# Kernel tuning notes

Measured on AMD Instinct MI355X. Metric: run time of the kernel, lower is better.

The kernel has to match this reference:

```python
import jax, jax.numpy as jnp
import numpy as np

B, Q, D = 8, 900, 256
NH, DH = 8, 32
FF = 1024
NLEVELS, NPOINTS, NLAYERS = 4, 4, 6
SHAPES = [(100, 100), (50, 50), (25, 25), (13, 13)]
S = sum(h * w for h, w in SHAPES)  # 13294
EPS = 1e-5
SCALE = 1.0 / float(np.sqrt(DH))


def layer_norm(x, g, b):
    mu = jnp.mean(x, -1, keepdims=True)
    var = jnp.var(x, -1, keepdims=True)
    return (x - mu) * jax.lax.rsqrt(var + EPS) * g + b


def mha(x, wi, bi, wo, bo):
    qkv = x @ wi.T + bi
    q, k, v = jnp.split(qkv, 3, axis=-1)
    q = q.reshape(B, Q, NH, DH)
    k = k.reshape(B, Q, NH, DH)
    v = v.reshape(B, Q, NH, DH)
    attn = jax.nn.softmax(jnp.einsum('bqhd,bkhd->bhqk', q, k) * SCALE, -1)
    o = jnp.einsum('bhqk,bkhd->bqhd', attn, v).reshape(B, Q, D)
    return o @ wo.T + bo


def msda_core(value, loc, aw):
    # value (B,S,NH,DH); loc (B,Q,NH,L,P,2) in [0,1]; aw (B,Q,NH,L,P)
    v = value.transpose(0, 2, 1, 3)  # (B,NH,S,DH)
    out = jnp.zeros((B, NH, Q, DH), value.dtype)
    start = 0
    for lvl, (H_, W_) in enumerate(SHAPES):
        vl = v[:, :, start:start + H_ * W_]  # (B,NH,HW,DH)
        start += H_ * W_
        l = loc[:, :, :, lvl].transpose(0, 2, 1, 3, 4).reshape(B, NH, Q * NPOINTS, 2)
        # grid_sample align_corners=False pixel coords
        x = l[..., 0] * W_ - 0.5
        y = l[..., 1] * H_ - 0.5
        x0 = jnp.floor(x)
        y0 = jnp.floor(y)
        wx = x - x0
        wy = y - y0
        g = jnp.zeros((B, NH, Q * NPOINTS, DH), value.dtype)
        for dy, dx, w in ((0, 0, (1 - wx) * (1 - wy)), (0, 1, wx * (1 - wy)),
                          (1, 0, (1 - wx) * wy), (1, 1, wx * wy)):
            xi = x0 + dx
            yi = y0 + dy
            valid = ((xi >= 0) & (xi < W_) & (yi >= 0) & (yi < H_)).astype(value.dtype)
            idx = (jnp.clip(yi, 0, H_ - 1) * W_ + jnp.clip(xi, 0, W_ - 1)).astype(jnp.int32)
            gi = jnp.take_along_axis(vl, idx[..., None], axis=2)  # (B,NH,QP,DH)
            g = g + gi * (w * valid)[..., None]
        g = g.reshape(B, NH, Q, NPOINTS, DH)
        a = aw[:, :, :, lvl].transpose(0, 2, 1, 3)  # (B,NH,Q,P)
        out = out + jnp.einsum('bhqpd,bhqp->bhqd', g, a)
    return out.transpose(0, 2, 1, 3).reshape(B, Q, D)


def msda(query, ref, value_in, vp_w, vp_b, so_w, so_b, aw_w, aw_b, op_w, op_b):
    value = (value_in @ vp_w.T + vp_b).reshape(B, S, NH, DH)
    off = (query @ so_w.T + so_b).reshape(B, Q, NH, NLEVELS, NPOINTS, 2)
    aw = (query @ aw_w.T + aw_b).reshape(B, Q, NH, NLEVELS * NPOINTS)
    aw = jax.nn.softmax(aw, -1).reshape(B, Q, NH, NLEVELS, NPOINTS)
    # offset normalizer is (W, H) per level
    norm = jnp.array([[w, h] for h, w in SHAPES], jnp.float32)
    loc = ref[:, :, None, :, None, :] + off / norm[None, None, None, :, None, :]
    return msda_core(value, loc, aw) @ op_w.T + op_b


def setup_inputs():
    key = jax.random.key(0)
    it = iter(jax.random.split(key, 32))

    def rn(shape, s=0.02):
        return jax.random.normal(next(it), shape, jnp.float32) * s

    z = lambda n: jnp.zeros((n,), jnp.float32)
    o = lambda n: jnp.ones((n,), jnp.float32)
    NOFF = NH * NLEVELS * NPOINTS
    return {
        'tgt': rn((B, Q, D), 1.0),
        'reference_points': jax.random.uniform(next(it), (B, Q, 2), jnp.float32),
        'memory': rn((B, S, D), 1.0),
        'spatial_shapes': jnp.array(SHAPES, jnp.int32),
        'level_start_index': jnp.array(np.cumsum([0] + [h * w for h, w in SHAPES[:-1]]), jnp.int32),
        'valid_ratios': jnp.ones((B, NLEVELS, 2), jnp.float32),
        'query_pos': rn((B, Q, D), 1.0),
        'sa_in_w': rn((3 * D, D)), 'sa_in_b': z(3 * D),
        'sa_out_w': rn((D, D)), 'sa_out_b': z(D),
        'n1_g': o(D), 'n1_b': z(D),
        'n2_g': o(D), 'n2_b': z(D),
        'n3_g': o(D), 'n3_b': z(D),
        'vp_w': rn((D, D)), 'vp_b': z(D),
        'so_w': rn((NOFF * 2, D)), 'so_b': rn((NOFF * 2,), 0.5),
        'aw_w': rn((NOFF, D)), 'aw_b': z(NOFF),
        'op_w': rn((D, D)), 'op_b': z(D),
        'ff1_w': rn((FF, D)), 'ff1_b': z(FF),
        'ff2_w': rn((D, FF)), 'ff2_b': z(D),
    }


def reference(tgt, reference_points, memory, spatial_shapes, level_start_index,
              valid_ratios, query_pos,
              sa_in_w, sa_in_b, sa_out_w, sa_out_b,
              n1_g, n1_b, n2_g, n2_b, n3_g, n3_b,
              vp_w, vp_b, so_w, so_b, aw_w, aw_b, op_w, op_b,
              ff1_w, ff1_b, ff2_w, ff2_b):
    # NOTE: nn.ModuleList([decoder_layer]*num_layers) in the source shares one
    # layer's weights across all 6 layers; bbox_embed is None so reference
    # points are constant across layers.
    output = tgt
    ref_input = reference_points[:, :, None, :] * valid_ratios[:, None, :, :]  # (B,Q,L,2)
    inter, inter_refs = [], []
    for _ in range(NLAYERS):
        output = output + query_pos
        t2 = mha(output, sa_in_w, sa_in_b, sa_out_w, sa_out_b)
        output = layer_norm(output + t2, n1_g, n1_b)
        t2 = msda(output, ref_input, memory, vp_w, vp_b, so_w, so_b, aw_w, aw_b, op_w, op_b)
        output = layer_norm(output + t2, n2_g, n2_b)
        t2 = jax.nn.relu(output @ ff1_w.T + ff1_b) @ ff2_w.T + ff2_b
        output = layer_norm(output + t2, n3_g, n3_b)
        inter.append(output)
        inter_refs.append(reference_points)
    return (jnp.stack(inter), jnp.stack(inter_refs))
```

## Files before the change

kernel.cpp:

```cpp
#include <hip/hip_runtime.h>
#include <hip/hip_bf16.h>

typedef __hip_bfloat16 bf16;
typedef __bf16 bf16x8 __attribute__((ext_vector_type(8)));
typedef float  f32x4  __attribute__((ext_vector_type(4)));

#define NB 8
#define NQ 900
#define DM 256
#define NHEADS 8
#define DHEAD 32
#define NFF 1024
#define NLAY 6
#define NS 13294
#define BQ (NB*NQ)
#define LN_EPS 1e-5f
#define ATT_SCALE 0.17677669529663687f
#define SAK 40
#define VWS 264

__device__ __forceinline__ float bfd(const bf16* p, size_t i){ return __bfloat162float(p[i]); }

__device__ __forceinline__ float ldv(const void* p, size_t i, int mode, bool extF32)
{
    if (mode == 0) return ((const float*)p)[i];
    if (mode == 1) return bfd((const bf16*)p, i);
    return extF32 ? ((const float*)p)[i] : bfd((const bf16*)p, i);
}

__device__ __forceinline__ void unpack8(uint4 u, float* t)
{
    t[0] = __uint_as_float((u.x & 0xffffu) << 16);
    t[1] = __uint_as_float(u.x & 0xffff0000u);
    t[2] = __uint_as_float((u.y & 0xffffu) << 16);
    t[3] = __uint_as_float(u.y & 0xffff0000u);
    t[4] = __uint_as_float((u.z & 0xffffu) << 16);
    t[5] = __uint_as_float(u.z & 0xffff0000u);
    t[6] = __uint_as_float((u.w & 0xffffu) << 16);
    t[7] = __uint_as_float(u.w & 0xffff0000u);
}

__global__ __launch_bounds__(256) void detect_dtype(const void* __restrict__ tgt,
        float* __restrict__ flag)
{
    __shared__ float red[256];
    int t = threadIdx.x;
    const unsigned short* u = (const unsigned short*)tgt;
    float m = 0.f;
    for (int i = t; i < 2048; i += 256) {
        unsigned int bits = ((unsigned int)u[i]) << 16;
        float v = fabsf(__uint_as_float(bits));
        if (!isfinite(v)) v = 1e30f;
        m = fmaxf(m, v);
    }
    red[t] = m;
    __syncthreads();
    for (int st = 128; st; st >>= 1) {
        if (t < st) red[t] = fmaxf(red[t], red[t + st]);
        __syncthreads();
    }
    if (t == 0) flag[0] = (red[0] > 1e8f) ? 1.f : 0.f;
}

__global__ __launch_bounds__(256) void convert_w(const void* __restrict__ src,
        bf16* __restrict__ dst, const float* __restrict__ flagp)
{
    const bool ef = flagp[0] > 0.5f;
    size_t base = ((size_t)blockIdx.x * 256 + threadIdx.x) * 8;
    if (ef) {
        const float* s = (const float*)src + base;
        float4 f0 = *(const float4*)s;
        float4 f1 = *(const float4*)(s + 4);
        union { bf16 a[8]; uint4 u; } t;
        t.a[0] = __float2bfloat16(f0.x); t.a[1] = __float2bfloat16(f0.y);
        t.a[2] = __float2bfloat16(f0.z); t.a[3] = __float2bfloat16(f0.w);
        t.a[4] = __float2bfloat16(f1.x); t.a[5] = __float2bfloat16(f1.y);
        t.a[6] = __float2bfloat16(f1.z); t.a[7] = __float2bfloat16(f1.w);
        *(uint4*)(dst + base) = t.u;
    } else {
        *(uint4*)(dst + base) = *(const uint4*)((const bf16*)src + base);
    }
}

__global__ __launch_bounds__(256) void gemm_vp(const void* __restrict__ A,
        const bf16* __restrict__ Wb, const void* __restrict__ bias,
        bf16* __restrict__ C, int M, const float* __restrict__ flagp)
{
    const bool ef = flagp[0] > 0.5f;
    __shared__ __align__(16) bf16 Wl[256 * VWS];
    __shared__ __align__(16) bf16 Al[32 * VWS];
    const int tid = threadIdx.x;
    const int w = tid >> 6, lane = tid & 63, lm = lane & 15, lq = lane >> 4;
    const int wq = w * 64;

    for (int u = tid; u < 8192; u += 256) {
        int row = u >> 5, col = (u & 31) * 8;
        *(uint4*)&Wl[row * VWS + col] = *(const uint4*)(Wb + (size_t)row * 256 + col);
    }

    float bv[4];
    #pragma unroll
    for (int nt = 0; nt < 4; nt++) bv[nt] = ldv(bias, wq + nt * 16 + lm, 2, ef);

    const int arow_l = tid >> 3;
    const int acol   = (tid & 7) * 32;

    const int ntiles = (M + 31) / 32;
    for (int tile = blockIdx.x; tile < ntiles; tile += gridDim.x) {
        const int m0 = tile * 32;
        __syncthreads();
        {
            const int grow = m0 + arow_l;
            if (grow < M) {
                if (ef) {
                    const float* ap = (const float*)A + (size_t)grow * 256 + acol;
                    #pragma unroll
                    for (int j = 0; j < 4; j++) {
                        float4 f0 = *(const float4*)(ap + j * 8);
                        float4 f1 = *(const float4*)(ap + j * 8 + 4);
                        union { bf16 a[8]; uint4 u; } t;
                        t.a[0] = __float2bfloat16(f0.x); t.a[1] = __float2bfloat16(f0.y);
                        t.a[2] = __float2bfloat16(f0.z); t.a[3] = __float2bfloat16(f0.w);
                        t.a[4] = __float2bfloat16(f1.x); t.a[5] = __float2bfloat16(f1.y);
                        t.a[6] = __float2bfloat16(f1.z); t.a[7] = __float2bfloat16(f1.w);
                        *(uint4*)&Al[arow_l * VWS + acol + j * 8] = t.u;
                    }
                } else {
                    const bf16* ap = (const bf16*)A + (size_t)grow * 256 + acol;
                    #pragma unroll
                    for (int j = 0; j < 4; j++)
                        *(uint4*)&Al[arow_l * VWS + acol + j * 8] =
                            *(const uint4*)(ap + j * 8);
                }
            } else {
                uint4 z = make_uint4(0u, 0u, 0u, 0u);
                #pragma unroll
                for (int j = 0; j < 4; j++)
                    *(uint4*)&Al[arow_l * VWS + acol + j * 8] = z;
            }
        }
        __syncthreads();

        f32x4 acc[2][4];
        #pragma unroll
        for (int mi = 0; mi < 2; mi++)
            #pragma unroll
            for (int nt = 0; nt < 4; nt++)
                acc[mi][nt] = (f32x4){0.f, 0.f, 0.f, 0.f};

        #pragma unroll
        for (int ks = 0; ks < 8; ks++) {
            bf16x8 af[2];
            #pragma unroll
            for (int mi = 0; mi < 2; mi++)
                af[mi] = *(const bf16x8*)&Al[(mi * 16 + lm) * VWS + ks * 32 + lq * 8];
            #pragma unroll
            for (int nt = 0; nt < 4; nt++) {
                bf16x8 bfr = *(const bf16x8*)&Wl[(wq + nt * 16 + lm) * VWS + ks * 32 + lq * 8];
                #pragma unroll
                for (int mi = 0; mi < 2; mi++)
                    acc[mi][nt] = __builtin_amdgcn_mfma_f32_16x16x32_bf16(
                                      af[mi], bfr, acc[mi][nt], 0, 0, 0);
            }
        }

        #pragma unroll
        for (int mi = 0; mi < 2; mi++) {
            #pragma unroll
            for (int r = 0; r < 4; r++) {
                int m = m0 + mi * 16 + lq * 4 + r;
                if (m >= M) continue;
                #pragma unroll
                for (int nt = 0; nt < 4; nt++) {
                    int col = wq + nt * 16 + lm;
                    C[(size_t)m * 256 + col] = __float2bfloat16(acc[mi][nt][r] + bv[nt]);
                }
            }
        }
    }
}

__device__ __forceinline__ void stage_a32(bf16* As, const void* A, bool a_bf16,
        int m0, int M, int K, int k0, int tid)
{
    const int row = tid >> 3, col = (tid & 7) * 4;
    const int arow = m0 + row;
    union { bf16 a[4]; uint2 u; } t;
    if (arow < M) {
        size_t base = (size_t)arow * K + k0 + col;
        if (a_bf16) {
            t.u = *(const uint2*)((const bf16*)A + base);
        } else {
            float4 f = *(const float4*)((const float*)A + base);
            t.a[0] = __float2bfloat16(f.x); t.a[1] = __float2bfloat16(f.y);
            t.a[2] = __float2bfloat16(f.z); t.a[3] = __float2bfloat16(f.w);
        }
    } else {
        t.u = make_uint2(0u, 0u);
    }
    *(uint2*)&As[row * SAK + col] = t.u;
}

__global__ __launch_bounds__(256) void gemm_a(const void* __restrict__ A, int amode,
        const bf16* __restrict__ Wb, const void* __restrict__ bias,
        void* __restrict__ C, int cmode, int M, int N, int K, int relu,
        const float* __restrict__ flagp)
{
    const bool ef = flagp[0] > 0.5f;
    const bool a_bf16 = (amode == 1) || (amode == 2 && !ef);
    __shared__ __align__(16) bf16 As[32 * SAK];
    __shared__ __align__(16) bf16 Ws[256 * SAK];
    const int tid = threadIdx.x;
    const int m0 = blockIdx.y * 32, n0 = blockIdx.x * 256;
    const int w = tid >> 6, lane = tid & 63, lm = lane & 15, lq = lane >> 4;
    const int wr = w >> 1, wc = w & 1;
    const int srow = tid >> 2, scol = (tid & 3) * 8;

    f32x4 acc[8];
    #pragma unroll
    for (int nt = 0; nt < 8; nt++) acc[nt] = (f32x4){0.f, 0.f, 0.f, 0.f};

    for (int k0 = 0; k0 < K; k0 += 32) {
        stage_a32(As, A, a_bf16, m0, M, K, k0, tid);
        #pragma unroll
        for (int it = 0; it < 4; it++) {
            int rr = it * 64 + srow;
            *(uint4*)&Ws[rr * SAK + scol] =
                *(const uint4*)(Wb + (size_t)(n0 + rr) * K + k0 + scol);
        }
        __syncthreads();

        bf16x8 af = *(const bf16x8*)&As[(wr * 16 + lm) * SAK + lq * 8];
        #pragma unroll
        for (int nt = 0; nt < 8; nt++) {
            bf16x8 bfr = *(const bf16x8*)&Ws[(wc * 128 + nt * 16 + lm) * SAK + lq * 8];
            acc[nt] = __builtin_amdgcn_mfma_f32_16x16x32_bf16(af, bfr, acc[nt], 0, 0, 0);
        }
        __syncthreads();
    }

    #pragma unroll
    for (int nt = 0; nt < 8; nt++) {
        int n = n0 + wc * 128 + nt * 16 + lm;
        float bv = ldv(bias, n, 2, ef);
        #pragma unroll
        for (int r = 0; r < 4; r++) {
            int m = m0 + wr * 16 + lq * 4 + r;
            if (m >= M) continue;
            float v = acc[nt][r] + bv;
            if (relu) v = fmaxf(v, 0.f);
            size_t ci = (size_t)m * N + n;
            if (cmode == 0) ((float*)C)[ci] = v;
            else            ((bf16*)C)[ci] = __float2bfloat16(v);
        }
    }
}

__global__ __launch_bounds__(256) void gemm_ln(const bf16* __restrict__ A,
        const bf16* __restrict__ Wb, const void* __restrict__ bias,
        const float* __restrict__ res, const void* __restrict__ gw,
        const void* __restrict__ bw, float* __restrict__ out32,
        bf16* __restrict__ outbf, void* __restrict__ dout, size_t obase,
        const void* __restrict__ qp, int M, int K,
        const float* __restrict__ flagp)
{
    const bool ef = flagp[0] > 0.5f;
    __shared__ __align__(16) bf16 As[32 * SAK];
    __shared__ __align__(16) bf16 Ws[256 * SAK];
    const int tid = threadIdx.x;
    const int m0 = blockIdx.y * 32;
    const int w = tid >> 6, lane = tid & 63, lm = lane & 15, lq = lane >> 4;
    const int wr = w >> 1, wc = w & 1;
    const int srow = tid >> 2, scol = (tid & 3) * 8;

    f32x4 acc[8];
    #pragma unroll
    for (int nt = 0; nt < 8; nt++) acc[nt] = (f32x4){0.f, 0.f, 0.f, 0.f};

    for (int k0 = 0; k0 < K; k0 += 32) {
        stage_a32(As, A, true, m0, M, K, k0, tid);
        #pragma unroll
        for (int it = 0; it < 4; it++) {
            int rr = it * 64 + srow;
            *(uint4*)&Ws[rr * SAK + scol] =
                *(const uint4*)(Wb + (size_t)rr * K + k0 + scol);
        }
        __syncthreads();

        bf16x8 af = *(const bf16x8*)&As[(wr * 16 + lm) * SAK + lq * 8];
        #pragma unroll
        for (int nt = 0; nt < 8; nt++) {
            bf16x8 bfr = *(const bf16x8*)&Ws[(wc * 128 + nt * 16 + lm) * SAK + lq * 8];
            acc[nt] = __builtin_amdgcn_mfma_f32_16x16x32_bf16(af, bfr, acc[nt], 0, 0, 0);
        }
        __syncthreads();
    }

    float bias_c[8], gcol[8], bcol[8];
    #pragma unroll
    for (int nt = 0; nt < 8; nt++) {
        int col = wc * 128 + nt * 16 + lm;
        bias_c[nt] = ldv(bias, col, 2, ef);
        gcol[nt]   = ldv(gw,   col, 2, ef);
        bcol[nt]   = ldv(bw,   col, 2, ef);
    }
    #pragma unroll
    for (int r = 0; r < 4; r++) {
        int row = m0 + wr * 16 + lq * 4 + r;
        bool vr_ = row < M;
        #pragma unroll
        for (int nt = 0; nt < 8; nt++) {
            int col = wc * 128 + nt * 16 + lm;
            float rv = vr_ ? res[(size_t)row * DM + col] : 0.f;
            acc[nt][r] += bias_c[nt] + rv;
        }
    }

    float* red = (float*)As;
    float mu[4], rstd[4];
    #pragma unroll
    for (int r = 0; r < 4; r++) {
        float s = 0.f;
        #pragma unroll
        for (int nt = 0; nt < 8; nt++) s += acc[nt][r];
        s += __shfl_xor(s, 1, 64); s += __shfl_xor(s, 2, 64);
        s += __shfl_xor(s, 4, 64); s += __shfl_xor(s, 8, 64);
        if (lm == 0) red[(wr * 16 + lq * 4 + r) * 2 + wc] = s;
    }
    __syncthreads();
    #pragma unroll
    for (int r = 0; r < 4; r++) {
        int rl = wr * 16 + lq * 4 + r;
        mu[r] = (red[rl * 2] + red[rl * 2 + 1]) * (1.f / DM);
    }
    #pragma unroll
    for (int r = 0; r < 4; r++) {
        float q = 0.f;
        #pragma unroll
        for (int nt = 0; nt < 8; nt++) {
            float d = acc[nt][r] - mu[r];
            q += d * d;
        }
        q += __shfl_xor(q, 1, 64); q += __shfl_xor(q, 2, 64);
        q += __shfl_xor(q, 4, 64); q += __shfl_xor(q, 8, 64);
        if (lm == 0) red[64 + (wr * 16 + lq * 4 + r) * 2 + wc] = q;
    }
    __syncthreads();
    #pragma unroll
    for (int r = 0; r < 4; r++) {
        int rl = wr * 16 + lq * 4 + r;
        float var = (red[64 + rl * 2] + red[64 + rl * 2 + 1]) * (1.f / DM);
        rstd[r] = rsqrtf(var + LN_EPS);
    }

    #pragma unroll
    for (int r = 0; r < 4; r++) {
        int row = m0 + wr * 16 + lq * 4 + r;
        if (row >= M) continue;
        size_t rbase = (size_t)row * DM;
        #pragma unroll
        for (int nt = 0; nt < 8; nt++) {
            int col = wc * 128 + nt * 16 + lm;
            float o = (acc[nt][r] - mu[r]) * rstd[r] * gcol[nt] + bcol[nt];
            if (dout) {
                if (ef) ((float*)dout)[obase + rbase + col] = o;
                else    ((bf16*)dout)[obase + rbase + col] = __float2bfloat16(o);
            }
            float o2 = o + (qp ? ldv(qp, rbase + col, 2, ef) : 0.f);
            out32[rbase + col] = o2;
            outbf[rbase + col] = __float2bfloat16(o2);
        }
    }
}

__global__ __launch_bounds__(256) void gemm_soaw(const bf16* __restrict__ A,
        const bf16* __restrict__ Wb, const void* __restrict__ b1,
        const void* __restrict__ b2, float* __restrict__ C1,
        float* __restrict__ C2, int M, const float* __restrict__ flagp)
{
    const bool ef = flagp[0] > 0.5f;
    const int K = DM;
    __shared__ __align__(16) bf16 As[32 * SAK];
    __shared__ __align__(16) bf16 Ws[128 * SAK];
    const int tid = threadIdx.x;
    const int m0 = blockIdx.y * 32, n0 = blockIdx.x * 128;
    const int w = tid >> 6, lane = tid & 63, lm = lane & 15, lq = lane >> 4;
    const int wr = w >> 1, wc = w & 1;
    const int srow = tid >> 2, scol = (tid & 3) * 8;

    f32x4 acc[4];
    #pragma unroll
    for (int nt = 0; nt < 4; nt++) acc[nt] = (f32x4){0.f, 0.f, 0.f, 0.f};

    for (int k0 = 0; k0 < K; k0 += 32) {
        stage_a32(As, A, true, m0, M, K, k0, tid);
        #pragma unroll
        for (int it = 0; it < 2; it++) {
            int rr = it * 64 + srow;
            *(uint4*)&Ws[rr * SAK + scol] =
                *(const uint4*)(Wb + (size_t)(n0 + rr) * K + k0 + scol);
        }
        __syncthreads();

        bf16x8 af = *(const bf16x8*)&As[(wr * 16 + lm) * SAK + lq * 8];
        #pragma unroll
        for (int nt = 0; nt < 4; nt++) {
            bf16x8 bfr = *(const bf16x8*)&Ws[(wc * 64 + nt * 16 + lm) * SAK + lq * 8];
            acc[nt] = __builtin_amdgcn_mfma_f32_16x16x32_bf16(af, bfr, acc[nt], 0, 0, 0);
        }
        __syncthreads();
    }

    float* Cd; const void* bsrc; int nst, c0;
    if (n0 < 256) { Cd = C1; bsrc = b1; nst = 256; c0 = n0; }
    else          { Cd = C2; bsrc = b2; nst = 128; c0 = n0 - 256; }

    #pragma unroll
    for (int nt = 0; nt < 4; nt++) {
        int cl = wc * 64 + nt * 16 + lm;
        float bv = ldv(bsrc, c0 + cl, 2, ef);
        #pragma unroll
        for (int r = 0; r < 4; r++) {
            int m = m0 + wr * 16 + lq * 4 + r;
            if (m >= M) continue;
            Cd[(size_t)m * nst + c0 + cl] = acc[nt][r] + bv;
        }
    }
}

__global__ __launch_bounds__(256) void add_qpos(const void* __restrict__ a, int amode,
        const void* __restrict__ qp, float* __restrict__ o, bf16* __restrict__ ob,
        const float* __restrict__ flagp)
{
    const bool ef = flagp[0] > 0.5f;
    int i = blockIdx.x * 256 + threadIdx.x;
    float v = ldv(a, i, amode, ef) + ldv(qp, i, 2, ef);
    o[i]  = v;
    ob[i] = __float2bfloat16(v);
}

__global__ __launch_bounds__(256) void mha_mfma(const bf16* __restrict__ qkv,
        bf16* __restrict__ out)
{
    const int qt = blockIdx.x, h = blockIdx.y, b = blockIdx.z;
    const int q0 = qt * 64;
    const int tid = threadIdx.x;
    const int w = tid >> 6, lane = tid & 63;
    const int lm = lane & 15, lq = lane >> 4;
    const int srow = tid >> 2, sc = (tid & 3) * 8;

    __shared__ __align__(16) bf16 Qs[64][SAK];
    __shared__ __align__(16) bf16 Ks[64][SAK];
    __shared__ __align__(16) bf16 Vt[32][66];
    __shared__ __align__(16) bf16 Pt[64][66];

    const bf16* base = qkv + (size_t)b * NQ * 768;

    {
        bf16 tmp[8];
        if (q0 + srow < NQ) {
            uint4 u = *(const uint4*)(base + (size_t)(q0 + srow) * 768 + h * DHEAD + sc);
            float t[8]; unpack8(u, t);
            #pragma unroll
            for (int i = 0; i < 8; i++) tmp[i] = __float2bfloat16(t[i] * ATT_SCALE);
        } else {
            #pragma unroll
            for (int i = 0; i < 8; i++) tmp[i] = __float2bfloat16(0.f);
        }
        *(uint4*)&Qs[srow][sc] = *(const uint4*)tmp;
    }
    __syncthreads();
    const bf16x8 qf = *(const bf16x8*)&Qs[w * 16 + lm][lq * 8];

    f32x4 O[2] = {{0.f,0.f,0.f,0.f},{0.f,0.f,0.f,0.f}};
    float mrow = -1e30f, lrow = 0.f;

    for (int k0 = 0; k0 < NQ; k0 += 64) {
        __syncthreads();
        {
            uint4 uk = {0u,0u,0u,0u}, uv = {0u,0u,0u,0u};
            if (k0 + srow < NQ) {
                const bf16* rp = base + (size_t)(k0 + srow) * 768 + h * DHEAD + sc;
                uk = *(const uint4*)(rp + 256);
                uv = *(const uint4*)(rp + 512);
            }
            *(uint4*)&Ks[srow][sc] = uk;
            const bf16* vv = (const bf16*)&uv;
            #pragma unroll
            for (int i = 0; i < 8; i++) Vt[sc + i][srow] = vv[i];
        }
        __syncthreads();

        float sv[16];
        #pragma unroll
        for (int mt = 0; mt < 4; mt++) {
            bf16x8 kf = *(const bf16x8*)&Ks[mt * 16 + lm][lq * 8];
            f32x4 d = __builtin_amdgcn_mfma_f32_16x16x32_bf16(kf, qf,
                        (f32x4){0.f,0.f,0.f,0.f}, 0, 0, 0);
            sv[mt*4+0] = d[0]; sv[mt*4+1] = d[1]; sv[mt*4+2] = d[2]; sv[mt*4+3] = d[3];
        }
        #pragma unroll
        for (int mt = 0; mt < 4; mt++)
            #pragma unroll
            for (int r = 0; r < 4; r++)
                if (k0 + mt * 16 + lq * 4 + r >= NQ) sv[mt*4+r] = -1e30f;

        float tmax = sv[0];
        #pragma unroll
        for (int j = 1; j < 16; j++) tmax = fmaxf(tmax, sv[j]);
        tmax = fmaxf(tmax, __shfl_xor(tmax, 16, 64));
        tmax = fmaxf(tmax, __shfl_xor(tmax, 32, 64));
        float mnew = fmaxf(mrow, tmax);
        float alpha = __expf(mrow - mnew);
        mrow = mnew;
        float psum = 0.f;
        #pragma unroll
        for (int j = 0; j < 16; j++) {
            float p = __expf(sv[j] - mnew);
            sv[j] = p; psum += p;
        }
        psum += __shfl_xor(psum, 16, 64);
        psum += __shfl_xor(psum, 32, 64);
        lrow = lrow * alpha + psum;

        #pragma unroll
        for (int mt = 0; mt < 4; mt++)
            #pragma unroll
            for (int r = 0; r < 4; r++)
                Pt[mt * 16 + lq * 4 + r][w * 16 + lm] = __float2bfloat16(sv[mt*4+r]);

        #pragma unroll
        for (int mt = 0; mt < 2; mt++)
            #pragma unroll
            for (int r = 0; r < 4; r++) O[mt][r] *= alpha;
        #pragma unroll
        for (int ks = 0; ks < 2; ks++) {
            union { bf16 a[8]; bf16x8 v; } pf;
            #pragma unroll
            for (int j = 0; j < 8; j++)
                pf.a[j] = Pt[ks * 32 + lq * 8 + j][w * 16 + lm];
            #pragma unroll
            for (int mt = 0; mt < 2; mt++) {
                bf16x8 vf = *(const bf16x8*)&Vt[mt * 16 + lm][ks * 32 + lq * 8];
                O[mt] = __builtin_amdgcn_mfma_f32_16x16x32_bf16(vf, pf.v, O[mt], 0, 0, 0);
            }
        }
    }

    int q = q0 + w * 16 + lm;
    if (q < NQ) {
        float invl = 1.f / lrow;
        bf16* op = out + ((size_t)(b * NQ + q)) * DM + h * DHEAD;
        #pragma unroll
        for (int mt = 0; mt < 2; mt++)
            #pragma unroll
            for (int r = 0; r < 4; r++)
                op[mt * 16 + lq * 4 + r] = __float2bfloat16(O[mt][r] * invl);
    }
}

__global__ __launch_bounds__(256) void msda_sample(const bf16* __restrict__ value,
        const float* __restrict__ off, const float* __restrict__ aw,
        const void* __restrict__ refp, const void* __restrict__ vr,
        bf16* __restrict__ out, const float* __restrict__ flagp)
{
    const bool ef = flagp[0] > 0.5f;
    int bq = blockIdx.x; int b = bq / NQ;
    int tid = threadIdx.x; int h = tid >> 5, d = tid & 31;
    __shared__ float sOff[256];
    __shared__ float sAw[128];
    __shared__ float sref[2];
    __shared__ float svr[8];
    sOff[tid] = off[(size_t)bq * 256 + tid];
    if (tid < 128) sAw[tid] = aw[(size_t)bq * 128 + tid];
    if (tid < 2)   sref[tid] = ldv(refp, bq * 2 + tid, 2, ef);
    if (tid < 8)   svr[tid]  = ldv(vr, b * 8 + tid, 2, ef);
    __syncthreads();
    if (tid < 8) {
        float* p = &sAw[tid * 16];
        float mx = -1e30f;
        #pragma unroll
        for (int j = 0; j < 16; j++) mx = fmaxf(mx, p[j]);
        float s = 0.f;
        #pragma unroll
        for (int j = 0; j < 16; j++) { float e = __expf(p[j] - mx); p[j] = e; s += e; }
        float inv = 1.f / s;
        #pragma unroll
        for (int j = 0; j < 16; j++) p[j] *= inv;
    }
    __syncthreads();
    const bf16* vb = value + (size_t)b * NS * DM + h * DHEAD + d;
    const int HS[4] = {100, 50, 25, 13};
    const int ST[4] = {0, 10000, 12500, 13125};
    float acc = 0.f;
    #pragma unroll
    for (int lvl = 0; lvl < 4; lvl++) {
        int W_ = HS[lvl], H_ = HS[lvl], st = ST[lvl];
        float rx = sref[0] * svr[lvl*2 + 0] * (float)W_;
        float ry = sref[1] * svr[lvl*2 + 1] * (float)H_;
        #pragma unroll
        for (int p = 0; p < 4; p++) {
            int oi = h * 32 + lvl * 8 + p * 2;
            float x = fminf(fmaxf(rx + sOff[oi]     - 0.5f, -4.f), (float)W_ + 4.f);
            float y = fminf(fmaxf(ry + sOff[oi + 1] - 0.5f, -4.f), (float)H_ + 4.f);
            float x0f = floorf(x), y0f = floorf(y);
            float wx = x - x0f, wy = y - y0f;
            int x0 = (int)x0f, y0 = (int)y0f;
            int x1i = x0 + 1, y1i = y0 + 1;
            bool vx0 = (x0 >= 0) && (x0 < W_), vx1 = (x1i >= 0) && (x1i < W_);
            bool vy0 = (y0 >= 0) && (y0 < H_), vy1 = (y1i >= 0) && (y1i < H_);
            float g = 0.f;
            if (vy0) {
                int rowo = (st + y0 * W_) * DM;
                if (vx0) g += (1.f - wx) * (1.f - wy) * __bfloat162float(vb[rowo + x0  * DM]);
                if (vx1) g += wx         * (1.f - wy) * __bfloat162float(vb[rowo + x1i * DM]);
            }
            if (vy1) {
                int rowo = (st + y1i * W_) * DM;
                if (vx0) g += (1.f - wx) * wy * __bfloat162float(vb[rowo + x0  * DM]);
                if (vx1) g += wx         * wy * __bfloat162float(vb[rowo + x1i * DM]);
            }
            acc += g * sAw[h * 16 + lvl * 4 + p];
        }
    }
    out[(size_t)bq * DM + tid] = __float2bfloat16(acc);
}

__global__ __launch_bounds__(256) void copy_refs(const void* __restrict__ refp,
        void* __restrict__ out, const float* __restrict__ flagp)
{
    const bool ef = flagp[0] > 0.5f;
    int i = blockIdx.x * 256 + threadIdx.x;
    if (i >= NLAY * BQ * 2) return;
    float v = ldv(refp, i % (BQ * 2), 2, ef);
    size_t oi = (size_t)NLAY * BQ * DM + i;
    if (ef) ((float*)out)[oi] = v;
    else    ((bf16*)out)[oi] = __float2bfloat16(v);
}

extern "C" void kernel_launch(void* const* d_in, const int* in_sizes, int n_in,
                              void* d_out, int out_size, void* d_ws, size_t ws_size,
                              hipStream_t stream)
{
    const void* tgt     = d_in[0];
    const void* refp    = d_in[1];
    const void* memory  = d_in[2];
    const void* vr      = d_in[5];
    const void* qp      = d_in[6];
    const void* sa_in_w = d_in[7];
    const void* sa_in_b = d_in[8];
    const void* sa_out_w= d_in[9];
    const void* sa_out_b= d_in[10];
    const void* n1_g    = d_in[11];
    const void* n1_b    = d_in[12];
    const void* n2_g    = d_in[13];
    const void* n2_b    = d_in[14];
    const void* n3_g    = d_in[15];
    const void* n3_b    = d_in[16];
    const void* vp_w    = d_in[17];
    const void* vp_b    = d_in[18];
    const void* so_w    = d_in[19];
    const void* so_b    = d_in[20];
    const void* aw_w    = d_in[21];
    const void* aw_b    = d_in[22];
    const void* op_w    = d_in[23];
    const void* op_b    = d_in[24];
    const void* ff1_w   = d_in[25];
    const void* ff1_b   = d_in[26];
    const void* ff2_w   = d_in[27];
    const void* ff2_b   = d_in[28];

    char* w = (char*)d_ws;
    float* flagp  = (float*)w;  w += 256;
    bf16*  value  = (bf16*)w;   w += (size_t)NB * NS * DM * 2;
    float* outbuf = (float*)w;  w += (size_t)BQ * DM * 4;
    float* x1samp = (float*)w;  w += (size_t)BQ * DM * 4;
    bf16*  bigb   = (bf16*)w;   w += (size_t)BQ * NFF * 2;
    float* attoff = (float*)w;  w += (size_t)BQ * DM * 4;
    float* awb    = (float*)w;  w += (size_t)BQ * 128 * 4;
    bf16*  abuf   = (bf16*)w;   w += (size_t)BQ * DM * 2;
    bf16*  outbf  = (bf16*)w;   w += (size_t)BQ * DM * 2;
    bf16* wb_sa_in = (bf16*)w;  w += (size_t)768 * 256 * 2;
    bf16* wb_sa_out= (bf16*)w;  w += (size_t)256 * 256 * 2;
    bf16* wb_soaw  = (bf16*)w;  w += (size_t)384 * 256 * 2;
    bf16* wb_op    = (bf16*)w;  w += (size_t)256 * 256 * 2;
    bf16* wb_ff1   = (bf16*)w;  w += (size_t)NFF * 256 * 2;
    bf16* wb_ff2   = (bf16*)w;  w += (size_t)256 * NFF * 2;
    bf16* wb_vp    = (bf16*)w;  w += (size_t)256 * 256 * 2;

    const int gy = (BQ + 31) / 32;
    const int MV = NB * NS;

    detect_dtype<<<1, 256, 0, stream>>>(tgt, flagp);
    convert_w<<< 96, 256, 0, stream>>>(sa_in_w,  wb_sa_in,  flagp);
    convert_w<<< 32, 256, 0, stream>>>(sa_out_w, wb_sa_out, flagp);
    convert_w<<< 32, 256, 0, stream>>>(so_w,     wb_soaw,   flagp);
    convert_w<<< 16, 256, 0, stream>>>(aw_w,     wb_soaw + 256 * 256, flagp);
    convert_w<<< 32, 256, 0, stream>>>(op_w,     wb_op,     flagp);
    convert_w<<<128, 256, 0, stream>>>(ff1_w,    wb_ff1,    flagp);
    convert_w<<<128, 256, 0, stream>>>(ff2_w,    wb_ff2,    flagp);
    convert_w<<< 32, 256, 0, stream>>>(vp_w,     wb_vp,     flagp);

    gemm_vp<<<256, 256, 0, stream>>>(memory, wb_vp, vp_b, value, MV, flagp);

    copy_refs<<<(NLAY * BQ * 2 + 255) / 256, 256, 0, stream>>>(refp, d_out, flagp);

    add_qpos<<<BQ * DM / 256, 256, 0, stream>>>(tgt, 2, qp, x1samp, abuf, flagp);

    for (int l = 0; l < NLAY; l++) {
        gemm_a<<<dim3(768/256, gy), 256, 0, stream>>>(
            abuf, 1, wb_sa_in, sa_in_b, bigb, 1, BQ, 768, DM, 0, flagp);
        mha_mfma<<<dim3(15, NHEADS, NB), 256, 0, stream>>>(bigb, abuf);
        gemm_ln<<<dim3(1, gy), 256, 0, stream>>>(
            abuf, wb_sa_out, sa_out_b, x1samp, n1_g, n1_b,
            outbuf, outbf, nullptr, 0, nullptr, BQ, DM, flagp);

        gemm_soaw<<<dim3(3, gy), 256, 0, stream>>>(
            outbf, wb_soaw, so_b, aw_b, attoff, awb, BQ, flagp);
        msda_sample<<<BQ, 256, 0, stream>>>(value, attoff, awb, refp, vr, abuf, flagp);
        gemm_ln<<<dim3(1, gy), 256, 0, stream>>>(
            abuf, wb_op, op_b, outbuf, n2_g, n2_b,
            outbuf, outbf, nullptr, 0, nullptr, BQ, DM, flagp);

        gemm_a<<<dim3(NFF/256, gy), 256, 0, stream>>>(
            outbf, 1, wb_ff1, ff1_b, bigb, 1, BQ, NFF, DM, 1, flagp);
        gemm_ln<<<dim3(1, gy), 256, 0, stream>>>(
            bigb, wb_ff2, ff2_b, outbuf, n3_g, n3_b,
            x1samp, abuf, d_out, (size_t)l * BQ * DM, qp, BQ, NFF, flagp);
    }
}
```

Before: 1.722 ms.

## Vectorize MSDA sampling with 8-channel loads and 8 queries per block

Rewrites the deformable-attention sampling kernel so that each thread handles 8 contiguous channels through 16-byte bf16 loads rather than one scalar channel. Each block now processes 8 queries, 32 threads per query, and stages the offsets and attention weights with float4 loads. The aim is fewer memory instructions for the gather and less per-block overhead, since the old launch used one block per query. The trade-off is more registers per thread and fewer threads in flight to hide gather latency. It also relies on an unpack8 helper and assumes BQ is divisible by 8, which holds here.

```diff
diff --git a/kernel.cpp b/kernel.cpp
--- a/kernel.cpp
+++ b/kernel.cpp
@@ -559,25 +559,41 @@
     }
 }
 
-__global__ __launch_bounds__(256) void msda_sample(const bf16* __restrict__ value,
+__global__ __launch_bounds__(256) void msda_sample8(const bf16* __restrict__ value,
         const float* __restrict__ off, const float* __restrict__ aw,
         const void* __restrict__ refp, const void* __restrict__ vr,
         bf16* __restrict__ out, const float* __restrict__ flagp)
 {
     const bool ef = flagp[0] > 0.5f;
-    int bq = blockIdx.x; int b = bq / NQ;
-    int tid = threadIdx.x; int h = tid >> 5, d = tid & 31;
-    __shared__ float sOff[256];
-    __shared__ float sAw[128];
-    __shared__ float sref[2];
-    __shared__ float svr[8];
-    sOff[tid] = off[(size_t)bq * 256 + tid];
-    if (tid < 128) sAw[tid] = aw[(size_t)bq * 128 + tid];
-    if (tid < 2)   sref[tid] = ldv(refp, bq * 2 + tid, 2, ef);
-    if (tid < 8)   svr[tid]  = ldv(vr, b * 8 + tid, 2, ef);
+    const int tid = threadIdx.x;
+    const int bq0 = blockIdx.x * 8;
+
+    __shared__ float sOff[8][256];
+    __shared__ float sAw[8][128];
+    __shared__ float sref[8][2];
+    __shared__ float svrq[8][8];
+
+    {
+        const float* osrc = off + (size_t)bq0 * 256;
+        #pragma unroll
+        for (int i = 0; i < 2; i++) {
+            int e = i * 1024 + tid * 4;
+            *(float4*)&sOff[e >> 8][e & 255] = *(const float4*)(osrc + e);
+        }
+        int e2 = tid * 4;
+        *(float4*)&sAw[e2 >> 7][e2 & 127] = *(const float4*)(aw + (size_t)bq0 * 128 + e2);
+    }
+    if (tid < 16) sref[tid >> 1][tid & 1] = ldv(refp, (size_t)(bq0 + (tid >> 1)) * 2 + (tid & 1), 2, ef);
+    if (tid < 64) {
+        int qi = tid >> 3, j = tid & 7;
+        int b = (bq0 + qi) / NQ;
+        svrq[qi][j] = ldv(vr, b * 8 + j, 2, ef);
+    }
     __syncthreads();
-    if (tid < 8) {
-        float* p = &sAw[tid * 16];
+
+    if (tid < 64) {
+        int qi = tid >> 3, h = tid & 7;
+        float* p = &sAw[qi][h * 16];
         float mx = -1e30f;
         #pragma unroll
         for (int j = 0; j < 16; j++) mx = fmaxf(mx, p[j]);
@@ -589,41 +605,83 @@
         for (int j = 0; j < 16; j++) p[j] *= inv;
     }
     __syncthreads();
-    const bf16* vb = value + (size_t)b * NS * DM + h * DHEAD + d;
+
+    const int qi = tid >> 5, sub = tid & 31;
+    const int h = sub >> 2, cg = sub & 3;
+    const int bq = bq0 + qi;
+    const int b = bq / NQ;
+    const bf16* vb = value + (size_t)b * NS * DM + h * DHEAD + cg * 8;
+
+    float acc[8];
+    #pragma unroll
+    for (int j = 0; j < 8; j++) acc[j] = 0.f;
+
     const int HS[4] = {100, 50, 25, 13};
     const int ST[4] = {0, 10000, 12500, 13125};
-    float acc = 0.f;
     #pragma unroll
     for (int lvl = 0; lvl < 4; lvl++) {
-        int W_ = HS[lvl], H_ = HS[lvl], st = ST[lvl];
-        float rx = sref[0] * svr[lvl*2 + 0] * (float)W_;
-        float ry = sref[1] * svr[lvl*2 + 1] * (float)H_;
+        const int W_ = HS[lvl], H_ = HS[lvl], st = ST[lvl];
+        float rx = sref[qi][0] * svrq[qi][lvl * 2 + 0] * (float)W_;
+        float ry = sref[qi][1] * svrq[qi][lvl * 2 + 1] * (float)H_;
         #pragma unroll
         for (int p = 0; p < 4; p++) {
             int oi = h * 32 + lvl * 8 + p * 2;
-            float x = fminf(fmaxf(rx + sOff[oi]     - 0.5f, -4.f), (float)W_ + 4.f);
-            float y = fminf(fmaxf(ry + sOff[oi + 1] - 0.5f, -4.f), (float)H_ + 4.f);
+            float x = fminf(fmaxf(rx + sOff[qi][oi]     - 0.5f, -4.f), (float)W_ + 4.f);
+            float y = fminf(fmaxf(ry + sOff[qi][oi + 1] - 0.5f, -4.f), (float)H_ + 4.f);
             float x0f = floorf(x), y0f = floorf(y);
             float wx = x - x0f, wy = y - y0f;
             int x0 = (int)x0f, y0 = (int)y0f;
             int x1i = x0 + 1, y1i = y0 + 1;
             bool vx0 = (x0 >= 0) && (x0 < W_), vx1 = (x1i >= 0) && (x1i < W_);
             bool vy0 = (y0 >= 0) && (y0 < H_), vy1 = (y1i >= 0) && (y1i < H_);
-            float g = 0.f;
+            float g[8];
+            #pragma unroll
+            for (int j = 0; j < 8; j++) g[j] = 0.f;
+            float t[8];
             if (vy0) {
                 int rowo = (st + y0 * W_) * DM;
-                if (vx0) g += (1.f - wx) * (1.f - wy) * __bfloat162float(vb[rowo + x0  * DM]);
-                if (vx1) g += wx         * (1.f - wy) * __bfloat162float(vb[rowo + x1i * DM]);
+                if (vx0) {
+                    uint4 u = *(const uint4*)(vb + rowo + x0 * DM);
+                    unpack8(u, t);
+                    float wgt = (1.f - wx) * (1.f - wy);
+                    #pragma unroll
+                    for (int j = 0; j < 8; j++) g[j] += wgt * t[j];
+                }
+                if (vx1) {
+                    uint4 u = *(const uint4*)(vb + rowo + x1i * DM);
+                    unpack8(u, t);
+                    float wgt = wx * (1.f - wy);
+                    #pragma unroll
+                    for (int j = 0; j < 8; j++) g[j] += wgt * t[j];
+                }
             }
             if (vy1) {
                 int rowo = (st + y1i * W_) * DM;
-                if (vx0) g += (1.f - wx) * wy * __bfloat162float(vb[rowo + x0  * DM]);
-                if (vx1) g += wx         * wy * __bfloat162float(vb[rowo + x1i * DM]);
+                if (vx0) {
+                    uint4 u = *(const uint4*)(vb + rowo + x0 * DM);
+                    unpack8(u, t);
+                    float wgt = (1.f - wx) * wy;
+                    #pragma unroll
+                    for (int j = 0; j < 8; j++) g[j] += wgt * t[j];
+                }
+                if (vx1) {
+                    uint4 u = *(const uint4*)(vb + rowo + x1i * DM);
+                    unpack8(u, t);
+                    float wgt = wx * wy;
+                    #pragma unroll
+                    for (int j = 0; j < 8; j++) g[j] += wgt * t[j];
+                }
             }
-            acc += g * sAw[h * 16 + lvl * 4 + p];
-        }
-    }
-    out[(size_t)bq * DM + tid] = __float2bfloat16(acc);
+            float a = sAw[qi][h * 16 + lvl * 4 + p];
+            #pragma unroll
+            for (int j = 0; j < 8; j++) acc[j] += a * g[j];
+        }
+    }
+
+    union { bf16 t[8]; uint4 u; } pk;
+    #pragma unroll
+    for (int j = 0; j < 8; j++) pk.t[j] = __float2bfloat16(acc[j]);
+    *(uint4*)(out + (size_t)bq * DM + h * DHEAD + cg * 8) = pk.u;
 }
 
 __global__ __launch_bounds__(256) void copy_refs(const void* __restrict__ refp,
@@ -717,7 +775,7 @@
 
         gemm_soaw<<<dim3(3, gy), 256, 0, stream>>>(
             outbf, wb_soaw, so_b, aw_b, attoff, awb, BQ, flagp);
-        msda_sample<<<BQ, 256, 0, stream>>>(value, attoff, awb, refp, vr, abuf, flagp);
+        msda_sample8<<<BQ / 8, 256, 0, stream>>>(value, attoff, awb, refp, vr, abuf, flagp);
         gemm_ln<<<dim3(1, gy), 256, 0, stream>>>(
             abuf, wb_op, op_b, outbuf, n2_g, n2_b,
             outbuf, outbf, nullptr, 0, nullptr, BQ, DM, flagp);
```

Measured after the change: 1.527 ms. -11.3%, faster.
